# Performance work log

Hardware: AMD Instinct MI355X
Metric: run time of the kernel (lower is better)

The kernel has to match this reference:

```python
import jax, jax.numpy as jnp
import numpy as np

N_SAMPLES = 1024   # self.n
B = 128            # batch of x
DIM = 64           # latent dim (self.dim)
DX = 64            # observation dim
K = 16             # annealing steps
N_LEAP = 3         # leapfrog inner steps
STEP = 0.05        # leapfrog step size
LOGVAR_P = 0.0     # momentum log-variance
LOG2PI = float(np.log(2.0 * np.pi))


def _betas():
    # beta_unnorm = sigmoid(4*(2*linspace(0,1,K+2)-1)); normalized to [0,1]
    b = jax.nn.sigmoid(4.0 * (2.0 * jnp.linspace(0.0, 1.0, K + 2) - 1.0))
    return (b - b[0]) / (b[-1] - b[0])


def _logprob_normal(z, logvar=0.0):
    return -0.5 * (LOG2PI + logvar + z * z * jnp.exp(-logvar))


def setup_inputs() -> dict:
    key = jax.random.key(0)
    k1, k2, k3, k4, k5 = jax.random.split(key, 5)
    x = jax.random.normal(k1, (B, DX), jnp.float32)
    W_enc = jax.random.normal(k2, (DX, DIM), jnp.float32) / jnp.sqrt(float(DX))
    W_dec = jax.random.normal(k3, (DIM, DX), jnp.float32) / jnp.sqrt(float(DIM))
    q_noise = jax.random.normal(k4, (N_SAMPLES, B, DIM), jnp.float32)
    p_noise = jax.random.normal(k5, (N_SAMPLES, B, DIM), jnp.float32)
    return {"x": x, "W_enc": W_enc, "W_dec": W_dec, "q_noise": q_noise, "p_noise": p_noise}


def reference(x, W_enc, W_dec, q_noise, p_noise):
    beta = _betas()
    mu = x @ W_enc  # (B, DIM) importance mean

    def loglik(q):  # Gaussian decoder logN(x | q @ W_dec, I), shape (n, B)
        r = jnp.einsum('nbd,de->nbe', q, W_dec)
        return _logprob_normal(x - r).sum(-1)

    def prior_lp(q):
        return _logprob_normal(q).sum(-1)

    def imp_lp(q):
        return _logprob_normal(q - mu).sum(-1)

    def w(q):  # functional: loglik + log prior - log importance
        return loglik(q) + prior_lp(q) - imp_lp(q)

    # initial samples from importance distr, initial momentum
    q0 = mu + q_noise                       # (n, B, DIM)
    p0 = jnp.exp(0.5 * LOGVAR_P) * p_noise  # (n, B, DIM)
    slw0 = (beta[1] - beta[0]) * w(q0)      # incremental weight at k=0

    noise_key = jax.random.key(42)

    def step(carry, inp):
        q, p, slw = carry
        bk, bkp1, kidx = inp
        # momentum refresh: v = 0 => full resample
        p = jnp.exp(0.5 * LOGVAR_P) * jax.random.normal(
            jax.random.fold_in(noise_key, kidx), q.shape, q.dtype)

        def tgt(qq):  # annealed target at beta_k (scalar for grad)
            return (bk * (loglik(qq) + prior_lp(qq)) + (1.0 - bk) * imp_lp(qq)).sum()

        g = jax.grad(tgt)
        for _ in range(N_LEAP):  # standard leapfrog
            p = p + 0.5 * STEP * g(q)
            q = q + STEP * p * jnp.exp(-LOGVAR_P)
            p = p + 0.5 * STEP * g(q)
        # NOTE: original torch accept/reject assignment is a no-op (chained
        # advanced indexing writes into a copy), so z_new is always kept.
        slw = slw + (bkp1 - bk) * w(q)
        return (q, p, slw), None

    ks = jnp.arange(1, K + 1)
    (qf, pf, slw), _ = jax.lax.scan(step, (q0, p0, slw0), (beta[1:K + 1], beta[2:K + 2], ks))
    return jax.scipy.special.logsumexp(slw, axis=0) - jnp.log(float(N_SAMPLES))
```

## Files before the change

kernel.cpp:

```cpp
#include <hip/hip_runtime.h>
#include <math.h>
#include <stdint.h>


#define WS_A     0
#define WS_MU    4096
#define WS_C     12288
#define WS_XSQ   20480
#define WS_AMU   20608
#define WS_F     28800
#define WS_WC    36992
#define WS_V     37120
#define WS_LAM   41216
#define WS_FZ    41280
#define WS_VF    49472
#define WS_SLW   53568
#define WS_FLG   (WS_SLW + 131072)
#define WS_RNG   (WS_FLG + 64)
#define WS_TOTAL WS_RNG
#define STEP_U32 8388608ull

#define LOG2PI 1.8378770664093453f

typedef _Float16 half8_t __attribute__((ext_vector_type(8)));
typedef float f4_t __attribute__((ext_vector_type(4)));
typedef unsigned int uint4_t __attribute__((ext_vector_type(4)));

struct KParams {
  float beta[18];
  float dbeta[17];
  uint32_t fk0[16];
  uint32_t fk1[16];
};

__host__ __device__ static inline void threefry2x32(uint32_t ks0, uint32_t ks1,
                                                    uint32_t x0, uint32_t x1,
                                                    uint32_t& o0, uint32_t& o1) {
  uint32_t ks2 = ks0 ^ ks1 ^ 0x1BD11BDAu;
  x0 += ks0; x1 += ks1;
#define TFR(r) { x0 += x1; x1 = (x1 << (r)) | (x1 >> (32 - (r))); x1 ^= x0; }
  TFR(13) TFR(15) TFR(26) TFR(6)
  x0 += ks1; x1 += ks2 + 1u;
  TFR(17) TFR(29) TFR(16) TFR(24)
  x0 += ks2; x1 += ks0 + 2u;
  TFR(13) TFR(15) TFR(26) TFR(6)
  x0 += ks0; x1 += ks1 + 3u;
  TFR(17) TFR(29) TFR(16) TFR(24)
  x0 += ks1; x1 += ks2 + 4u;
  TFR(13) TFR(15) TFR(26) TFR(6)
  x0 += ks2; x1 += ks0 + 5u;
#undef TFR
  o0 = x0; o1 = x1;
}

__device__ __forceinline__ float u_from_bits(uint32_t bits) {
  const float LO = __uint_as_float(0xBF7FFFFFu);
  float f = __uint_as_float((bits >> 9) | 0x3F800000u) - 1.0f;
  return fmaf(f, 2.0f, LO);
}

__device__ __forceinline__ float erfinv_f(float x) {
  float w = -__logf(fmaf(-x, x, 1.0f));
  float p;
  if (w < 5.0f) {
    w -= 2.5f;
    p = 2.81022636e-08f;
    p = fmaf(p, w, 3.43273939e-07f);
    p = fmaf(p, w, -3.5233877e-06f);
    p = fmaf(p, w, -4.39150654e-06f);
    p = fmaf(p, w, 0.00021858087f);
    p = fmaf(p, w, -0.00125372503f);
    p = fmaf(p, w, -0.00417768164f);
    p = fmaf(p, w, 0.246640727f);
    p = fmaf(p, w, 1.50140941f);
  } else {
    w = sqrtf(w) - 3.0f;
    p = -0.000200214257f;
    p = fmaf(p, w, 0.000100950558f);
    p = fmaf(p, w, 0.00134934322f);
    p = fmaf(p, w, -0.00367342844f);
    p = fmaf(p, w, 0.00573950773f);
    p = fmaf(p, w, -0.0076224613f);
    p = fmaf(p, w, 0.00943887047f);
    p = fmaf(p, w, 1.00167406f);
    p = fmaf(p, w, 2.83297682f);
  }
  return p * x;
}

__global__ void k_setup1(const float* __restrict__ x, const float* __restrict__ Wenc,
                         const float* __restrict__ Wdec, float* __restrict__ ws) {
  int t = blockIdx.x * 256 + threadIdx.x;
  if (t < 4096) {
    int i = t >> 6, j = t & 63;
    float s = 0;
    for (int e = 0; e < 64; ++e) s = fmaf(Wdec[i*64+e], Wdec[j*64+e], s);
    ws[WS_A + t] = s;
  } else if (t < 12288) {
    int u = t - 4096; int b = u >> 6, d = u & 63;
    float s = 0;
    for (int e = 0; e < 64; ++e) s = fmaf(x[b*64+e], Wenc[e*64+d], s);
    ws[WS_MU + u] = s;
  } else if (t < 20480) {
    int u = t - 12288; int b = u >> 6, d = u & 63;
    float s = 0;
    for (int e = 0; e < 64; ++e) s = fmaf(x[b*64+e], Wdec[d*64+e], s);
    ws[WS_C + u] = s;
  } else if (t < 20608) {
    int b = t - 20480;
    float s = 0;
    for (int e = 0; e < 64; ++e) s = fmaf(x[b*64+e], x[b*64+e], s);
    ws[WS_XSQ + b] = s;
  } else if (t == 20700) {
    ((int*)ws)[WS_FLG] = 0;
  }
}

#define DRAW(PC, IDX)                                                        \
  { uint32_t o0, o1;                                                         \
    threefry2x32(k0, k1, 0u, base + (IDX), o0, o1);                          \
    PC = 1.41421356f * erfinv_f(u_from_bits(o0 ^ o1)); }

#define PACKD(DST, DD)                                                       \
  { _Float16 hh = (_Float16)(DD);                                            \
    _Float16 ll = (_Float16)((DD) - (float)hh);                              \
    DST = (uint32_t)__builtin_bit_cast(unsigned short, hh) |                 \
          ((uint32_t)__builtin_bit_cast(unsigned short, ll) << 16); }

#define EP 65
__global__ __launch_bounds__(1024) void k_fused(float* __restrict__ ws, KParams P,
                                                int nRng, int nS, int Lcut) {
  const int blk = blockIdx.x;
  const int tid = threadIdx.x;
  if (blk == 0) {
    __shared__ float Am[64 * EP];
    __shared__ float Vm[64 * EP];
    __shared__ float cs_c[32], cs_s[32];
    __shared__ int ppu[32], ppv[32];
    for (int i = tid; i < 4096; i += 1024) {
      int r = i >> 6, c = i & 63;
      Am[r*EP + c] = ws[WS_A + i];
      Vm[r*EP + c] = (r == c) ? 1.0f : 0.0f;
    }
    const int pA = tid & 31;
    int uA = (pA == 0) ? 0 : pA;
    int vA = (pA == 0) ? 63 : (63 - pA);
    const int pV0 = tid >> 6;
    int uV0 = (pV0 == 0) ? 0 : pV0;
    int vV0 = (pV0 == 0) ? 63 : (63 - pV0);
    const int pV1 = 16 + pV0;
    int uV1 = pV1;
    int vV1 = 63 - pV1;
    __syncthreads();
    for (int sweep = 0; sweep < 3; ++sweep) {
      for (int r = 0; r < 63; ++r) {
        if (tid < 32) {
          float app = Am[uA*(EP+1)], aqq = Am[vA*(EP+1)], apq = Am[uA*EP+vA];
          float c = 1.0f, s = 0.0f;
          if (fabsf(apq) > 1e-30f) {
            float tau = (aqq - app) / (2.0f * apq);
            float t = copysignf(1.0f / (fabsf(tau) + sqrtf(fmaf(tau, tau, 1.0f))), tau);
            c = 1.0f / sqrtf(fmaf(t, t, 1.0f));
            s = t * c;
          }
          ppu[tid] = uA; ppv[tid] = vA; cs_c[tid] = c; cs_s[tid] = s;
        }
        __syncthreads();
        {
          int i = tid >> 5;
          int ui = ppu[i], vi = ppv[i];
          const int uj = uA, vj = vA;
          float ci = cs_c[i], si = cs_s[i], cj = cs_c[pA], sj = cs_s[pA];
          float a = Am[ui*EP+uj], bb = Am[ui*EP+vj];
          float d = Am[vi*EP+uj], e  = Am[vi*EP+vj];
          float r0u = ci*a  - si*d;
          float r1u = fmaf(si, a,  ci*d);
          float r0v = ci*bb - si*e;
          float r1v = fmaf(si, bb, ci*e);
          Am[ui*EP+uj] = cj*r0u - sj*r0v;
          Am[ui*EP+vj] = fmaf(sj, r0u, cj*r0v);
          Am[vi*EP+uj] = cj*r1u - sj*r1v;
          Am[vi*EP+vj] = fmaf(sj, r1u, cj*r1v);
        }
        {
          const int k = tid & 63;
          {
            float c2 = cs_c[pV0], s2 = cs_s[pV0];
            float vu = Vm[k*EP+uV0], vv = Vm[k*EP+vV0];
            Vm[k*EP+uV0] = c2*vu - s2*vv;
            Vm[k*EP+vV0] = fmaf(s2, vu, c2*vv);
          }
          {
            float c2 = cs_c[pV1], s2 = cs_s[pV1];
            float vu = Vm[k*EP+uV1], vv = Vm[k*EP+vV1];
            Vm[k*EP+uV1] = c2*vu - s2*vv;
            Vm[k*EP+vV1] = fmaf(s2, vu, c2*vv);
          }
        }
        uA  = (uA  == 0) ? 0 : ((uA  == 63) ? 1 : uA  + 1);
        vA  = (vA  == 63) ? 1 : vA  + 1;
        uV0 = (uV0 == 0) ? 0 : ((uV0 == 63) ? 1 : uV0 + 1);
        vV0 = (vV0 == 63) ? 1 : vV0 + 1;
        uV1 = (uV1 == 63) ? 1 : uV1 + 1;
        vV1 = (vV1 == 63) ? 1 : vV1 + 1;
        __syncthreads();
      }
    }
    if (tid < 64) ws[WS_LAM + tid] = Am[tid*(EP+1)];
    if (tid == 0) {
      while (atomicAdd((int*)ws + WS_FLG, 0) < 8) { }
    }
    __syncthreads();
    __threadfence();
    for (int t2 = tid; t2 < 8192; t2 += 1024) {
      int b = t2 >> 6, d = t2 & 63;
      float s = 0;
      for (int m = 0; m < 64; ++m) s = fmaf(ws[WS_F + b*64+m], Vm[m*EP+d], s);
      ws[WS_FZ + t2] = s;
    }
    {
      int idx = tid;
      int lane = idx & 63, Fr = idx >> 6;
      int t = Fr >> 3, kt = (Fr >> 2) & 1, nt = Fr & 3;
      int n = nt*16 + (lane & 15);
      int k0 = kt*32 + ((lane >> 4) & 3)*8;
      uint32_t out[4];
      for (int jj = 0; jj < 4; ++jj) {
        float v0 = Vm[(k0 + 2*jj    )*EP + n];
        float v1 = Vm[(k0 + 2*jj + 1)*EP + n];
        _Float16 h0, h1;
        if (t == 0) { h0 = (_Float16)v0; h1 = (_Float16)v1; }
        else {
          _Float16 a0 = (_Float16)v0, a1 = (_Float16)v1;
          h0 = (_Float16)(v0 - (float)a0);
          h1 = (_Float16)(v1 - (float)a1);
        }
        unsigned short u0 = __builtin_bit_cast(unsigned short, h0);
        unsigned short u1 = __builtin_bit_cast(unsigned short, h1);
        out[jj] = (uint32_t)u0 | ((uint32_t)u1 << 16);
      }
      uint32_t* dst = (uint32_t*)ws + WS_VF + idx*4;
      dst[0] = out[0]; dst[1] = out[1]; dst[2] = out[2]; dst[3] = out[3];
    }
    if (tid < 128) {
      int b = tid;
      float muc = 0, musq = 0, muamu = 0;
      for (int d = 0; d < 64; ++d) {
        float m = ws[WS_MU + b*64+d];
        muc   = fmaf(m, ws[WS_C + b*64+d], muc);
        musq  = fmaf(m, m, musq);
        muamu = fmaf(m, ws[WS_AMU + b*64+d], muamu);
      }
      ws[WS_WC + b] = -32.0f * LOG2PI - 0.5f * ws[WS_XSQ + b]
                      + muc - 0.5f * musq - 0.5f * muamu;
    }
  } else if (blk <= nRng) {
    const int L = (blk - 1) * 1024 + tid;
    const int bI = L >> 8, t256 = L & 255;
    const int wv = t256 >> 6, lane = t256 & 63;
    const int cw = lane & 15, g4 = lane >> 4;
    const int koff = g4 * 8;
    const int trajBase = bI * 64 + wv * 16;
    const uint32_t base = (uint32_t)(trajBase + cw) * 64u;
    uint32_t* wsu = (uint32_t*)ws;
    const int nSteps = nS + ((nS < 16 && L < Lcut) ? 1 : 0);
    for (int j = 1; j <= nSteps; ++j) {
      const uint32_t k0 = P.fk0[j-1], k1 = P.fk1[j-1];
      uint32_t ov[16];
#pragma unroll
      for (int i = 0; i < 8; ++i) { float dd; DRAW(dd, koff + i) PACKD(ov[i], dd) }
#pragma unroll
      for (int i = 0; i < 8; ++i) { float dd; DRAW(dd, 32 + koff + i) PACKD(ov[8+i], dd) }
      uint4_t* wr = (uint4_t*)(wsu + WS_RNG + (size_t)(j-1)*STEP_U32 + (size_t)L*16u);
      wr[0] = (uint4_t){ov[0], ov[1], ov[2], ov[3]};
      wr[1] = (uint4_t){ov[4], ov[5], ov[6], ov[7]};
      wr[2] = (uint4_t){ov[8], ov[9], ov[10], ov[11]};
      wr[3] = (uint4_t){ov[12], ov[13], ov[14], ov[15]};
    }
  } else {
    int t = (blk - 1 - nRng) * 1024 + tid;
    if (t < 8192) {
      int b = t >> 6, d = t & 63;
      float s = 0;
      for (int m = 0; m < 64; ++m) s = fmaf(ws[WS_MU + b*64+m], ws[WS_A + m*64+d], s);
      ws[WS_AMU + t] = s;
      ws[WS_F + t] = ws[WS_C + t] - ws[WS_MU + t] - s;
    }
    __syncthreads();
    if (tid == 0) {
      __threadfence();
      atomicAdd((int*)ws + WS_FLG, 1);
    }
  }
}


#define SPLIT1(AH, AL, J, VV)                                                \
  { _Float16 hh = (_Float16)(VV); AH[J] = hh;                                \
    AL[J] = (_Float16)((VV) - (float)hh); }

#define DRAWSPLIT8(AH, AL, KB)                                               \
  { float dd;                                                                \
    DRAW(dd, (KB)+0) SPLIT1(AH, AL, 0, dd)                                   \
    DRAW(dd, (KB)+1) SPLIT1(AH, AL, 1, dd)                                   \
    DRAW(dd, (KB)+2) SPLIT1(AH, AL, 2, dd)                                   \
    DRAW(dd, (KB)+3) SPLIT1(AH, AL, 3, dd)                                   \
    DRAW(dd, (KB)+4) SPLIT1(AH, AL, 4, dd)                                   \
    DRAW(dd, (KB)+5) SPLIT1(AH, AL, 5, dd)                                   \
    DRAW(dd, (KB)+6) SPLIT1(AH, AL, 6, dd)                                   \
    DRAW(dd, (KB)+7) SPLIT1(AH, AL, 7, dd) }

#define FRAGB(T, KT, NT)                                                     \
  __builtin_bit_cast(half8_t, VF[(((T)*2+(KT))*4+(NT))*64 + lane])

#define ROT1(ZO, NT, AH0, AL0, AH1, AL1)                                     \
  { half8_t bh0 = FRAGB(0,0,NT), bh1 = FRAGB(0,1,NT);                        \
    half8_t bl0 = FRAGB(1,0,NT), bl1 = FRAGB(1,1,NT);                        \
    f4_t aa = {0.f, 0.f, 0.f, 0.f};                                          \
    aa = __builtin_amdgcn_mfma_f32_16x16x32_f16(AH0, bh0, aa, 0, 0, 0);      \
    aa = __builtin_amdgcn_mfma_f32_16x16x32_f16(AH1, bh1, aa, 0, 0, 0);      \
    aa = __builtin_amdgcn_mfma_f32_16x16x32_f16(AL0, bh0, aa, 0, 0, 0);      \
    aa = __builtin_amdgcn_mfma_f32_16x16x32_f16(AL1, bh1, aa, 0, 0, 0);      \
    aa = __builtin_amdgcn_mfma_f32_16x16x32_f16(AH0, bl0, aa, 0, 0, 0);      \
    aa = __builtin_amdgcn_mfma_f32_16x16x32_f16(AH1, bl1, aa, 0, 0, 0);      \
    ZO = aa; }

#define ROTATE4(O0, O1, O2, O3, AH0, AL0, AH1, AL1)                          \
  ROT1(O0, 0, AH0, AL0, AH1, AL1) ROT1(O1, 1, AH0, AL0, AH1, AL1)            \
  ROT1(O2, 2, AH0, AL0, AH1, AL1) ROT1(O3, 3, AH0, AL0, AH1, AL1)

#define LF4V(ZV, PV, NLM, FV, DBL)                                           \
  { f4_t gg = __builtin_elementwise_fma(bk4,                                 \
        __builtin_elementwise_fma(NLM, ZV, FV), -ZV);                        \
    PV = __builtin_elementwise_fma(c025v, gg, PV);                           \
    if (DBL) PV = __builtin_elementwise_fma(c025v, gg, PV);                  \
    ZV = __builtin_elementwise_fma(c005v, PV, ZV); }
#define SUBSTEPV(DBL)                                                        \
  LF4V(z0, pz0, nlm0, fzv0, DBL) LF4V(z1, pz1, nlm1, fzv1, DBL)              \
  LF4V(z2, pz2, nlm2, fzv2, DBL) LF4V(z3, pz3, nlm3, fzv3, DBL)

#define W_EVALN(WOUT)                                                        \
  { f4_t s1 = fzv0*z0 + fzv1*z1 + fzv2*z2 + fzv3*z3;                         \
    f4_t s2 = (lmS0*z0)*z0 + (lmS1*z1)*z1 + (lmS2*z2)*z2 + (lmS3*z3)*z3;     \
    f4_t vv = s1 - 0.5f*s2;                                                  \
    float r0 = vv.x, r1 = vv.y, r2 = vv.z, r3 = vv.w;                        \
    r0 += __shfl_xor(r0, 1); r1 += __shfl_xor(r1, 1);                        \
    r2 += __shfl_xor(r2, 1); r3 += __shfl_xor(r3, 1);                        \
    r0 += __shfl_xor(r0, 2); r1 += __shfl_xor(r1, 2);                        \
    r2 += __shfl_xor(r2, 2); r3 += __shfl_xor(r3, 2);                        \
    r0 += __shfl_xor(r0, 4); r1 += __shfl_xor(r1, 4);                        \
    r2 += __shfl_xor(r2, 4); r3 += __shfl_xor(r3, 4);                        \
    r0 += __shfl_xor(r0, 8); r1 += __shfl_xor(r1, 8);                        \
    r2 += __shfl_xor(r2, 8); r3 += __shfl_xor(r3, 8);                        \
    float wsel = (cw == 0) ? r0 : ((cw == 1) ? r1 : ((cw == 2) ? r2 : r3));  \
    WOUT = wsel + wcs; }

#define PLO 0x05040100u
#define PHI 0x07060302u

__global__ __launch_bounds__(256) void k_main(const float* __restrict__ qn,
                                              const float* __restrict__ ws,
                                              float* __restrict__ slw_out,
                                              KParams P, int nS, int Lcut) {
  __shared__ uint4_t VF[1024];
  const int tid = threadIdx.x;
  {
    const uint4_t* src = (const uint4_t*)((const uint32_t*)ws + WS_VF);
    for (int i = tid; i < 1024; i += 256) VF[i] = src[i];
  }
  __syncthreads();

  const int lane = tid & 63;
  const int wv = tid >> 6;
  const int cw = lane & 15;
  const int g4 = lane >> 4;
  const int koff = g4 * 8;
  const int trajBase = blockIdx.x * 64 + wv * 16;
  const uint32_t base = (uint32_t)(trajBase + cw) * 64u;
  const int Lme = blockIdx.x * 256 + tid;

  const int b0 = (trajBase + g4*4 + 0) & 127;
  const int b1 = (trajBase + g4*4 + 1) & 127;
  const int b2 = (trajBase + g4*4 + 2) & 127;
  const int b3 = (trajBase + g4*4 + 3) & 127;
  f4_t fzv0, fzv1, fzv2, fzv3;
  fzv0.x = ws[WS_FZ + b0*64 + cw];      fzv0.y = ws[WS_FZ + b1*64 + cw];
  fzv0.z = ws[WS_FZ + b2*64 + cw];      fzv0.w = ws[WS_FZ + b3*64 + cw];
  fzv1.x = ws[WS_FZ + b0*64 + 16 + cw]; fzv1.y = ws[WS_FZ + b1*64 + 16 + cw];
  fzv1.z = ws[WS_FZ + b2*64 + 16 + cw]; fzv1.w = ws[WS_FZ + b3*64 + 16 + cw];
  fzv2.x = ws[WS_FZ + b0*64 + 32 + cw]; fzv2.y = ws[WS_FZ + b1*64 + 32 + cw];
  fzv2.z = ws[WS_FZ + b2*64 + 32 + cw]; fzv2.w = ws[WS_FZ + b3*64 + 32 + cw];
  fzv3.x = ws[WS_FZ + b0*64 + 48 + cw]; fzv3.y = ws[WS_FZ + b1*64 + 48 + cw];
  fzv3.z = ws[WS_FZ + b2*64 + 48 + cw]; fzv3.w = ws[WS_FZ + b3*64 + 48 + cw];
  const float lmS0 = ws[WS_LAM + cw];
  const float lmS1 = ws[WS_LAM + 16 + cw];
  const float lmS2 = ws[WS_LAM + 32 + cw];
  const float lmS3 = ws[WS_LAM + 48 + cw];
  const float wcs = ws[WS_WC + ((trajBase + g4*4 + (cw & 3)) & 127)];
  const f4_t nlm0 = {-lmS0, -lmS0, -lmS0, -lmS0};
  const f4_t nlm1 = {-lmS1, -lmS1, -lmS1, -lmS1};
  const f4_t nlm2 = {-lmS2, -lmS2, -lmS2, -lmS2};
  const f4_t nlm3 = {-lmS3, -lmS3, -lmS3, -lmS3};
  const f4_t c025v = {0.025f, 0.025f, 0.025f, 0.025f};
  const f4_t c005v = {0.05f, 0.05f, 0.05f, 0.05f};

  f4_t z0, z1, z2, z3, pz0, pz1, pz2, pz3;
  float slw = 0.0f;

  {
    const float* qp = qn + (size_t)base;
    f4_t qa = *(const f4_t*)(qp + koff);
    f4_t qb = *(const f4_t*)(qp + koff + 4);
    f4_t qc = *(const f4_t*)(qp + 32 + koff);
    f4_t qd = *(const f4_t*)(qp + 32 + koff + 4);
    half8_t ah0, al0, ah1, al1;
    SPLIT1(ah0, al0, 0, qa.x) SPLIT1(ah0, al0, 1, qa.y)
    SPLIT1(ah0, al0, 2, qa.z) SPLIT1(ah0, al0, 3, qa.w)
    SPLIT1(ah0, al0, 4, qb.x) SPLIT1(ah0, al0, 5, qb.y)
    SPLIT1(ah0, al0, 6, qb.z) SPLIT1(ah0, al0, 7, qb.w)
    SPLIT1(ah1, al1, 0, qc.x) SPLIT1(ah1, al1, 1, qc.y)
    SPLIT1(ah1, al1, 2, qc.z) SPLIT1(ah1, al1, 3, qc.w)
    SPLIT1(ah1, al1, 4, qd.x) SPLIT1(ah1, al1, 5, qd.y)
    SPLIT1(ah1, al1, 6, qd.z) SPLIT1(ah1, al1, 7, qd.w)
    ROTATE4(z0, z1, z2, z3, ah0, al0, ah1, al1)
  }
  {
    float w0;
    W_EVALN(w0);
    slw = fmaf(P.dbeta[0], w0, slw);
  }

  for (int j = 1; j <= 16; ++j) {
    const float bk = P.beta[j];
    const f4_t bk4 = {bk, bk, bk, bk};
    half8_t ah0, al0, ah1, al1;
    if (j <= nS || (j == nS + 1 && Lme < Lcut)) {
      const uint32_t* rp = (const uint32_t*)ws + WS_RNG
                         + (size_t)(j-1)*STEP_U32 + (size_t)Lme*16u;
      const uint4_t* rr = (const uint4_t*)rp;
      uint4_t q0 = rr[0], q1 = rr[1], q2 = rr[2], q3 = rr[3];
      uint4_t uh0 = { __builtin_amdgcn_perm(q0.y, q0.x, PLO),
                      __builtin_amdgcn_perm(q0.w, q0.z, PLO),
                      __builtin_amdgcn_perm(q1.y, q1.x, PLO),
                      __builtin_amdgcn_perm(q1.w, q1.z, PLO) };
      uint4_t ul0 = { __builtin_amdgcn_perm(q0.y, q0.x, PHI),
                      __builtin_amdgcn_perm(q0.w, q0.z, PHI),
                      __builtin_amdgcn_perm(q1.y, q1.x, PHI),
                      __builtin_amdgcn_perm(q1.w, q1.z, PHI) };
      uint4_t uh1 = { __builtin_amdgcn_perm(q2.y, q2.x, PLO),
                      __builtin_amdgcn_perm(q2.w, q2.z, PLO),
                      __builtin_amdgcn_perm(q3.y, q3.x, PLO),
                      __builtin_amdgcn_perm(q3.w, q3.z, PLO) };
      uint4_t ul1 = { __builtin_amdgcn_perm(q2.y, q2.x, PHI),
                      __builtin_amdgcn_perm(q2.w, q2.z, PHI),
                      __builtin_amdgcn_perm(q3.y, q3.x, PHI),
                      __builtin_amdgcn_perm(q3.w, q3.z, PHI) };
      ah0 = __builtin_bit_cast(half8_t, uh0);
      al0 = __builtin_bit_cast(half8_t, ul0);
      ah1 = __builtin_bit_cast(half8_t, uh1);
      al1 = __builtin_bit_cast(half8_t, ul1);
    } else {
      const uint32_t k0 = P.fk0[j-1], k1 = P.fk1[j-1];
      DRAWSPLIT8(ah0, al0, koff)
      DRAWSPLIT8(ah1, al1, 32 + koff)
    }
    ROTATE4(pz0, pz1, pz2, pz3, ah0, al0, ah1, al1)
    SUBSTEPV(false)
    SUBSTEPV(true)
    SUBSTEPV(true)
    float wj;
    W_EVALN(wj);
    slw = fmaf(P.dbeta[j], wj, slw);
  }
  if (cw < 4) slw_out[trajBase + g4*4 + cw] = slw;
}

__global__ void k_reduce(const float* __restrict__ slw, float* __restrict__ out) {
  __shared__ float red[256];
  int b = blockIdx.x, t = threadIdx.x;
  float v0 = slw[t*128 + b];
  float v1 = slw[(t+256)*128 + b];
  float v2 = slw[(t+512)*128 + b];
  float v3 = slw[(t+768)*128 + b];
  float m = fmaxf(fmaxf(v0, v1), fmaxf(v2, v3));
  red[t] = m; __syncthreads();
  for (int s = 128; s > 0; s >>= 1) {
    if (t < s) red[t] = fmaxf(red[t], red[t+s]);
    __syncthreads();
  }
  m = red[0]; __syncthreads();
  float sum = expf(v0 - m) + expf(v1 - m) + expf(v2 - m) + expf(v3 - m);
  red[t] = sum; __syncthreads();
  for (int s = 128; s > 0; s >>= 1) {
    if (t < s) red[t] += red[t+s];
    __syncthreads();
  }
  if (t == 0) out[b] = m + logf(red[0]) - 6.93147180559945309f;
}

extern "C" void kernel_launch(void* const* d_in, const int* in_sizes, int n_in,
                              void* d_out, int out_size, void* d_ws, size_t ws_size,
                              hipStream_t stream) {
  const float* x    = (const float*)d_in[0];
  const float* Wenc = (const float*)d_in[1];
  const float* Wdec = (const float*)d_in[2];
  const float* qn   = (const float*)d_in[3];
  float* ws  = (float*)d_ws;
  float* out = (float*)d_out;
  if (ws_size < (size_t)WS_TOTAL * sizeof(float)) return;

  size_t avail_u32 = ws_size / 4;
  int nS = 0, Lcut = 0;
  if (avail_u32 > (size_t)WS_RNG) {
    size_t r = avail_u32 - (size_t)WS_RNG;
    nS = (int)(r / STEP_U32);
    if (nS > 16) nS = 16;
    if (nS < 16) {
      size_t rem = r - (size_t)nS * STEP_U32;
      size_t lc = (rem / 16) & ~(size_t)63;
      if (lc > 524288) lc = 524288;
      Lcut = (int)lc;
    }
  }
  const int nRng = (nS > 0 || Lcut > 0) ? 512 : 0;

  KParams P;
  double bb[18];
  for (int i = 0; i < 18; ++i) {
    double tt = (double)i / 17.0;
    bb[i] = 1.0 / (1.0 + exp(-(8.0 * tt - 4.0)));
  }
  for (int i = 0; i < 18; ++i) P.beta[i] = (float)((bb[i] - bb[0]) / (bb[17] - bb[0]));
  for (int j = 0; j <= 16; ++j) P.dbeta[j] = P.beta[j+1] - P.beta[j];
  for (int k = 1; k <= 16; ++k) {
    uint32_t a, c;
    threefry2x32(0u, 42u, 0u, (uint32_t)k, a, c);
    P.fk0[k-1] = a; P.fk1[k-1] = c;
  }

  hipLaunchKernelGGL(k_setup1, dim3(81), dim3(256), 0, stream, x, Wenc, Wdec, ws);
  hipLaunchKernelGGL(k_fused, dim3(1 + nRng + 8), dim3(1024), 0, stream, ws, P, nRng, nS, Lcut);
  hipLaunchKernelGGL(k_main, dim3(2048), dim3(256), 0, stream, qn, ws, ws + WS_SLW, P, nS, Lcut);
  hipLaunchKernelGGL(k_reduce, dim3(128), dim3(256), 0, stream, ws + WS_SLW, out);
}
```

Before: 583.8 us.

## Move post-eigendecomposition setup work from eigen block to the eight helper blocks

The eigendecomposition block now writes V to global workspace and signals a second flag instead of waiting on the helper blocks and running the FZ matmul, V fp16 split packing and WC constant itself. The eight helper blocks wait on both flags, then split the FZ product across themselves, with block 0 packing VF and block 1 computing WC. This shortens the serial tail after the Jacobi sweep by spreading the work across blocks. It adds a global round-trip for V and a spin-wait in the helper blocks, which assumes all blocks are co-resident.

```diff
diff --git a/kernel.cpp b/kernel.cpp
--- a/kernel.cpp
+++ b/kernel.cpp
@@ -113,6 +113,8 @@
     ws[WS_XSQ + b] = s;
   } else if (t == 20700) {
     ((int*)ws)[WS_FLG] = 0;
+  } else if (t == 20701) {
+    ((int*)ws)[WS_FLG + 1] = 0;
   }
 }
 
@@ -206,54 +208,11 @@
         __syncthreads();
       }
     }
+    for (int i = tid; i < 4096; i += 1024) ws[WS_V + i] = Vm[(i >> 6)*EP + (i & 63)];
     if (tid < 64) ws[WS_LAM + tid] = Am[tid*(EP+1)];
-    if (tid == 0) {
-      while (atomicAdd((int*)ws + WS_FLG, 0) < 8) { }
-    }
+    __threadfence();
     __syncthreads();
-    __threadfence();
-    for (int t2 = tid; t2 < 8192; t2 += 1024) {
-      int b = t2 >> 6, d = t2 & 63;
-      float s = 0;
-      for (int m = 0; m < 64; ++m) s = fmaf(ws[WS_F + b*64+m], Vm[m*EP+d], s);
-      ws[WS_FZ + t2] = s;
-    }
-    {
-      int idx = tid;
-      int lane = idx & 63, Fr = idx >> 6;
-      int t = Fr >> 3, kt = (Fr >> 2) & 1, nt = Fr & 3;
-      int n = nt*16 + (lane & 15);
-      int k0 = kt*32 + ((lane >> 4) & 3)*8;
-      uint32_t out[4];
-      for (int jj = 0; jj < 4; ++jj) {
-        float v0 = Vm[(k0 + 2*jj    )*EP + n];
-        float v1 = Vm[(k0 + 2*jj + 1)*EP + n];
-        _Float16 h0, h1;
-        if (t == 0) { h0 = (_Float16)v0; h1 = (_Float16)v1; }
-        else {
-          _Float16 a0 = (_Float16)v0, a1 = (_Float16)v1;
-          h0 = (_Float16)(v0 - (float)a0);
-          h1 = (_Float16)(v1 - (float)a1);
-        }
-        unsigned short u0 = __builtin_bit_cast(unsigned short, h0);
-        unsigned short u1 = __builtin_bit_cast(unsigned short, h1);
-        out[jj] = (uint32_t)u0 | ((uint32_t)u1 << 16);
-      }
-      uint32_t* dst = (uint32_t*)ws + WS_VF + idx*4;
-      dst[0] = out[0]; dst[1] = out[1]; dst[2] = out[2]; dst[3] = out[3];
-    }
-    if (tid < 128) {
-      int b = tid;
-      float muc = 0, musq = 0, muamu = 0;
-      for (int d = 0; d < 64; ++d) {
-        float m = ws[WS_MU + b*64+d];
-        muc   = fmaf(m, ws[WS_C + b*64+d], muc);
-        musq  = fmaf(m, m, musq);
-        muamu = fmaf(m, ws[WS_AMU + b*64+d], muamu);
-      }
-      ws[WS_WC + b] = -32.0f * LOG2PI - 0.5f * ws[WS_XSQ + b]
-                      + muc - 0.5f * musq - 0.5f * muamu;
-    }
+    if (tid == 0) atomicAdd((int*)ws + WS_FLG + 1, 1);
   } else if (blk <= nRng) {
     const int L = (blk - 1) * 1024 + tid;
     const int bI = L >> 8, t256 = L & 255;
@@ -278,18 +237,64 @@
       wr[3] = (uint4_t){ov[12], ov[13], ov[14], ov[15]};
     }
   } else {
-    int t = (blk - 1 - nRng) * 1024 + tid;
-    if (t < 8192) {
+    const int sblk = blk - 1 - nRng;
+    int t = sblk * 1024 + tid;
+    {
       int b = t >> 6, d = t & 63;
       float s = 0;
       for (int m = 0; m < 64; ++m) s = fmaf(ws[WS_MU + b*64+m], ws[WS_A + m*64+d], s);
       ws[WS_AMU + t] = s;
       ws[WS_F + t] = ws[WS_C + t] - ws[WS_MU + t] - s;
     }
+    __threadfence();
     __syncthreads();
     if (tid == 0) {
-      __threadfence();
       atomicAdd((int*)ws + WS_FLG, 1);
+      while (atomicAdd((int*)ws + WS_FLG, 0) < 8 ||
+             atomicAdd((int*)ws + WS_FLG + 1, 0) < 1) { }
+    }
+    __syncthreads();
+    __threadfence();
+    {
+      int b = t >> 6, d = t & 63;
+      float s = 0;
+      for (int m = 0; m < 64; ++m) s = fmaf(ws[WS_F + b*64+m], ws[WS_V + m*64+d], s);
+      ws[WS_FZ + t] = s;
+    }
+    if (sblk == 0) {
+      int idx = tid;
+      int lane = idx & 63, Fr = idx >> 6;
+      int tt = Fr >> 3, kt = (Fr >> 2) & 1, nt = Fr & 3;
+      int n = nt*16 + (lane & 15);
+      int k0 = kt*32 + ((lane >> 4) & 3)*8;
+      uint32_t out[4];
+      for (int jj = 0; jj < 4; ++jj) {
+        float v0 = ws[WS_V + (k0 + 2*jj    )*64 + n];
+        float v1 = ws[WS_V + (k0 + 2*jj + 1)*64 + n];
+        _Float16 h0, h1;
+        if (tt == 0) { h0 = (_Float16)v0; h1 = (_Float16)v1; }
+        else {
+          _Float16 a0 = (_Float16)v0, a1 = (_Float16)v1;
+          h0 = (_Float16)(v0 - (float)a0);
+          h1 = (_Float16)(v1 - (float)a1);
+        }
+        unsigned short u0 = __builtin_bit_cast(unsigned short, h0);
+        unsigned short u1 = __builtin_bit_cast(unsigned short, h1);
+        out[jj] = (uint32_t)u0 | ((uint32_t)u1 << 16);
+      }
+      uint32_t* dst = (uint32_t*)ws + WS_VF + idx*4;
+      dst[0] = out[0]; dst[1] = out[1]; dst[2] = out[2]; dst[3] = out[3];
+    } else if (sblk == 1 && tid < 128) {
+      int b = tid;
+      float muc = 0, musq = 0, muamu = 0;
+      for (int d = 0; d < 64; ++d) {
+        float m = ws[WS_MU + b*64+d];
+        muc   = fmaf(m, ws[WS_C + b*64+d], muc);
+        musq  = fmaf(m, m, musq);
+        muamu = fmaf(m, ws[WS_AMU + b*64+d], muamu);
+      }
+      ws[WS_WC + b] = -32.0f * LOG2PI - 0.5f * ws[WS_XSQ + b]
+                      + muc - 0.5f * musq - 0.5f * muamu;
     }
   }
 }
```

New measurement: 565.1 us. 3.2% less time.
